# Performance work log

Measured on AMD Instinct MI355X. Metric: run time of the kernel, lower is better.

Reference implementation:

```python
import jax, jax.numpy as jnp
import numpy as np

B, S, D, E, H, K = 4, 2048, 1024, 8, 1024, 2


def setup_inputs() -> dict:
    key = jax.random.key(0)
    k0, k1, k2, k3 = jax.random.split(key, 4)
    x = jax.random.normal(k0, (B, S, D), dtype=jnp.float32)
    router_w = jax.random.normal(k1, (E, D), dtype=jnp.float32) * 0.02
    w1 = jax.random.normal(k2, (D, E * H), dtype=jnp.float32) * 0.02
    w2 = jax.random.normal(k3, (E * H, D), dtype=jnp.float32) * 0.02
    expert_bias = jnp.zeros((E,), dtype=jnp.float32)
    return {"x": x, "router_w": router_w, "w1": w1, "w2": w2, "expert_bias": expert_bias}


def reference(x, router_w, w1, w2, expert_bias):
    b, s, d = x.shape
    e = router_w.shape[0]
    x_flat = x.reshape(-1, d)                      # [T, D]
    T = x_flat.shape[0]

    # Router: sigmoid scores, bias-balanced top-k selection
    router_logits = x_flat @ router_w.T            # [T, E]
    router_probs = jax.nn.sigmoid(router_logits.astype(jnp.float32))
    selection_scores = router_probs + expert_bias[None, :]
    _, selected = jax.lax.top_k(selection_scores, K)          # [T, K] indices
    top_k_w = jnp.take_along_axis(router_probs, selected, axis=-1)
    top_k_w = top_k_w / (top_k_w.sum(-1, keepdims=True) + 1e-20)
    top_k_w = top_k_w.astype(x.dtype)

    # Combine weights as a sparse [T, E] matrix (equivalent to the
    # padded_gather / grouped-GEMM / padded_scatter pipeline since
    # unselected experts get weight 0).
    combine = jnp.zeros((T, e), dtype=x.dtype).at[
        jnp.arange(T)[:, None], selected].add(top_k_w)

    # Expert MLP: relu(x @ w1)^2 @ w2, experts are contiguous column blocks
    h = jnp.square(jax.nn.relu(x_flat @ w1))       # [T, E*H]
    h = h.reshape(T, e, H) * combine[:, :, None]   # weighted per-expert hidden
    y = jnp.einsum('teh,ehd->td', h, w2.reshape(e, H, d))
    output = y.reshape(b, s, d)

    # Aux losses
    router_z_loss = jnp.mean(jnp.square(jax.nn.logsumexp(router_logits, axis=-1)))
    sel_flat = selected.reshape(-1)
    tokens_per_expert = jnp.zeros((e,), jnp.float32).at[sel_flat].add(1.0)
    f_i = (tokens_per_expert / tokens_per_expert.sum()).astype(x.dtype)

    # bias-balancing branch: per-sequence load balance loss
    sel_seq = selected.reshape(b, s * K)
    f_seq = jnp.zeros((b, e), jnp.float32).at[
        jnp.arange(b)[:, None], sel_seq].add(1.0) / (s * K)
    p_seq = router_probs.reshape(b, s, e).mean(axis=1)
    load_balance_loss = e * (f_seq * p_seq).sum(-1).mean()

    # uniform expert widths -> normalized widths are all 1
    widths_norm = jnp.ones((e,), jnp.float32)
    compute_loss = (router_probs @ widths_norm).mean()

    return output, router_z_loss, load_balance_loss, compute_loss, f_i
```

## Files before the change

### kernel.cpp

```cpp
#include <hip/hip_runtime.h>

typedef unsigned short u16;
typedef unsigned int u32;
typedef __bf16 bf16x8 __attribute__((ext_vector_type(8)));
typedef float f32x4 __attribute__((ext_vector_type(4)));

#define NTOK   8192
#define DDIM   1024
#define NEXP   8
#define HDIM   1024
#define PAIRS  16384

__device__ __forceinline__ u16 f2bf(float f) {
  union { float f; u32 u; } v; v.f = f;
  u32 r = v.u + 0x7FFFu + ((v.u >> 16) & 1u);
  return (u16)(r >> 16);
}

__device__ __forceinline__ f32x4 mfma16(bf16x8 a, bf16x8 b, f32x4 c) {
  return __builtin_amdgcn_mfma_f32_16x16x32_bf16(a, b, c, 0, 0, 0);
}

__device__ __forceinline__ void gload16(const void* g, void* l) {
  __builtin_amdgcn_global_load_lds(
      (__attribute__((address_space(1))) void*)g,
      (__attribute__((address_space(3))) void*)l, 16, 0, 0);
}

__global__ __launch_bounds__(256) void transpose_cast(const float* __restrict__ in,
                                                      u16* __restrict__ out,
                                                      int R, int C,
                                                      long in_zs, long out_zs) {
  __shared__ float tile[32][33];
  long ib = (long)blockIdx.z * in_zs;
  long ob = (long)blockIdx.z * out_zs;
  int r0 = blockIdx.y * 32, c0 = blockIdx.x * 32;
  int tx = threadIdx.x & 31, ty = threadIdx.x >> 5;
  #pragma unroll
  for (int rr = 0; rr < 32; rr += 8)
    tile[ty + rr][tx] = in[ib + (long)(r0 + ty + rr) * C + c0 + tx];
  __syncthreads();
  #pragma unroll
  for (int rr = 0; rr < 32; rr += 8)
    out[ob + (long)(c0 + ty + rr) * R + r0 + tx] = f2bf(tile[tx][ty + rr]);
}

__global__ __launch_bounds__(256) void router_kernel(
    const float* __restrict__ x, const float* __restrict__ rw,
    const float* __restrict__ ebias, u16* __restrict__ xb,
    int2* __restrict__ sel, float2* __restrict__ selw,
    float* __restrict__ probs_t, float* __restrict__ lse2_buf,
    u32* __restrict__ cnt, u32* __restrict__ cnt_be) {
  __shared__ float rw_lds[8 * 1028];
  __shared__ double lg[16][8][2];
  __shared__ u32 cl[8];
  int tid = threadIdx.x;
  int tl = tid >> 4, e = (tid >> 1) & 7, s = tid & 1;
  int t = blockIdx.x * 16 + tl;

  for (int i = tid; i < 8192; i += 256)
    rw_lds[(i >> 10) * 1028 + (i & 1023)] = rw[i];
  if (tid < 8) cl[tid] = 0;
  __syncthreads();

  const float* xr = x + (long)t * DDIM;
  const float* wr = rw_lds + e * 1028;
  u16* xbr = xb + (long)t * DDIM;
  double a0 = 0.0, a1 = 0.0;
  int dbase = s * 512;
  for (int d0 = dbase; d0 < dbase + 512; d0 += 16) {
    float4 x0 = *(const float4*)(xr + d0);
    float4 w0 = *(const float4*)(wr + d0);
    float4 x1 = *(const float4*)(xr + d0 + 4);
    float4 w1v = *(const float4*)(wr + d0 + 4);
    float4 x2 = *(const float4*)(xr + d0 + 8);
    float4 w2v = *(const float4*)(wr + d0 + 8);
    float4 x3 = *(const float4*)(xr + d0 + 12);
    float4 w3 = *(const float4*)(wr + d0 + 12);
    a0 += (double)x0.x * w0.x + (double)x0.y * w0.y + (double)x0.z * w0.z + (double)x0.w * w0.w;
    a1 += (double)x1.x * w1v.x + (double)x1.y * w1v.y + (double)x1.z * w1v.z + (double)x1.w * w1v.w;
    a0 += (double)x2.x * w2v.x + (double)x2.y * w2v.y + (double)x2.z * w2v.z + (double)x2.w * w2v.w;
    a1 += (double)x3.x * w3.x + (double)x3.y * w3.y + (double)x3.z * w3.z + (double)x3.w * w3.w;
    if (e == 0) {
      *(ushort4*)(xbr + d0)     = make_ushort4(f2bf(x0.x), f2bf(x0.y), f2bf(x0.z), f2bf(x0.w));
      *(ushort4*)(xbr + d0 + 4) = make_ushort4(f2bf(x1.x), f2bf(x1.y), f2bf(x1.z), f2bf(x1.w));
      *(ushort4*)(xbr + d0 + 8) = make_ushort4(f2bf(x2.x), f2bf(x2.y), f2bf(x2.z), f2bf(x2.w));
      *(ushort4*)(xbr + d0 +12) = make_ushort4(f2bf(x3.x), f2bf(x3.y), f2bf(x3.z), f2bf(x3.w));
    }
  }
  lg[tl][e][s] = a0 + a1;
  __syncthreads();

  if (tid < 16) {
    int t2 = blockIdx.x * 16 + tid;
    double logit[8]; float p[8]; float score[8];
    for (int ee = 0; ee < 8; ee++) {
      logit[ee] = lg[tid][ee][0] + lg[tid][ee][1];
      p[ee] = (float)(1.0 / (1.0 + exp(-logit[ee])));
      score[ee] = p[ee] + ebias[ee];
      probs_t[ee * NTOK + t2] = p[ee];
    }
    int i0 = 0;
    for (int ee = 1; ee < 8; ee++) if (score[ee] > score[i0]) i0 = ee;
    int i1 = (i0 == 0) ? 1 : 0;
    for (int ee = 0; ee < 8; ee++) if (ee != i0 && score[ee] > score[i1]) i1 = ee;
    float w0 = p[i0], w1 = p[i1];
    float ssum = w0 + w1 + 1e-20f;
    sel[t2] = make_int2(i0, i1);
    selw[t2] = make_float2(w0 / ssum, w1 / ssum);
    double m = logit[0];
    for (int ee = 1; ee < 8; ee++) m = fmax(m, logit[ee]);
    double se = 0.0;
    for (int ee = 0; ee < 8; ee++) se += exp(logit[ee] - m);
    double ls = m + log(se);
    lse2_buf[t2] = (float)(ls * ls);
    atomicAdd(&cl[i0], 1u); atomicAdd(&cl[i1], 1u);
  }
  __syncthreads();
  if (tid < 8) {
    int b = (blockIdx.x * 16) >> 11;
    atomicAdd(&cnt[tid], cl[tid]);
    atomicAdd(&cnt_be[b * 8 + tid], cl[tid]);
  }
}

__global__ void offsets_kernel(const u32* __restrict__ cnt, u32* __restrict__ offs,
                               u32* __restrict__ cursor) {
  if (threadIdx.x == 0 && blockIdx.x == 0) {
    u32 a = 0;
    for (int e = 0; e < 8; e++) { offs[e] = a; cursor[e] = a; a += cnt[e]; }
  }
}

__global__ __launch_bounds__(256) void build_lists(
    const int2* __restrict__ sel, const float2* __restrict__ selw,
    u32* __restrict__ cursor, int* __restrict__ tok_list, float* __restrict__ wt_list,
    int* __restrict__ inv) {
  int t = blockIdx.x * 256 + threadIdx.x;
  int2 s = sel[t]; float2 w = selw[t];
  u32 p0 = atomicAdd(&cursor[s.x], 1u);
  tok_list[p0] = t; wt_list[p0] = w.x; inv[2 * t] = (int)p0;
  u32 p1 = atomicAdd(&cursor[s.y], 1u);
  tok_list[p1] = t; wt_list[p1] = w.y; inv[2 * t + 1] = (int)p1;
}

template <bool SECOND>
__global__ __launch_bounds__(256) void moe_gemm(
    const u16* __restrict__ A, const u16* __restrict__ Bt,
    u16* __restrict__ out16,
    const int* __restrict__ tok_list, const float* __restrict__ wt_list,
    const u32* __restrict__ cnt, const u32* __restrict__ offs) {
  int tn = blockIdx.x & 7;
  int tm = blockIdx.x >> 3;
  int e = 0, acct = 0;
  while (e < 8) {
    int nt = (int)((cnt[e] + 127u) >> 7);
    if (tm < acct + nt) break;
    acct += nt; e++;
  }
  if (e == 8) return;
  int m0 = (tm - acct) * 128;
  int off = (int)offs[e];
  int ce  = (int)cnt[e];

  __shared__ uint4 As[1024];
  __shared__ uint4 Bs[1024];

  int tid = threadIdx.x;
  int l = tid & 63, w = tid >> 6;

  const u16* agp[4]; const u16* bgp[4];
  #pragma unroll
  for (int j = 0; j < 4; j++) {
    int p = w * 256 + j * 64 + l;
    int row = p >> 3, c = p & 7;
    long arow;
    if (SECOND) {
      arow = (long)(off + m0 + row);
    } else {
      int rr = m0 + row; if (rr > ce - 1) rr = ce - 1;
      arow = (long)tok_list[off + rr];
    }
    agp[j] = A + arow * 1024 + c * 8;
    bgp[j] = Bt + (long)e * 1048576 + (long)(tn * 128 + row) * 1024 + c * 8;
  }

  f32x4 acc[4][4];
  #pragma unroll
  for (int i = 0; i < 4; i++)
    #pragma unroll
    for (int j = 0; j < 4; j++) acc[i][j] = (f32x4){0.f, 0.f, 0.f, 0.f};

  int mr = l & 15, q = l >> 4;
  int wm = (w >> 1) * 64, wn = (w & 1) * 64;

  for (int k0 = 0; k0 < 1024; k0 += 64) {
    #pragma unroll
    for (int j = 0; j < 4; j++) {
      gload16(agp[j], &As[w * 256 + j * 64]);
      gload16(bgp[j], &Bs[w * 256 + j * 64]);
      agp[j] += 64; bgp[j] += 64;
    }
    __syncthreads();
    #pragma unroll
    for (int kk = 0; kk < 2; kk++) {
      int cg = kk * 4 + q;
      bf16x8 af[4], bfr[4];
      #pragma unroll
      for (int i = 0; i < 4; i++) {
        af[i]  = __builtin_bit_cast(bf16x8, As[(wm + i * 16 + mr) * 8 + cg]);
        bfr[i] = __builtin_bit_cast(bf16x8, Bs[(wn + i * 16 + mr) * 8 + cg]);
      }
      #pragma unroll
      for (int i = 0; i < 4; i++)
        #pragma unroll
        for (int j = 0; j < 4; j++)
          acc[i][j] = mfma16(af[i], bfr[j], acc[i][j]);
    }
    __syncthreads();
  }

  #pragma unroll
  for (int i = 0; i < 4; i++) {
    #pragma unroll
    for (int r = 0; r < 4; r++) {
      int rr = wm + i * 16 + q * 4 + r;
      if (m0 + rr >= ce) continue;
      int slot = off + m0 + rr;
      float wgt = SECOND ? wt_list[slot] : 0.f;
      #pragma unroll
      for (int j = 0; j < 4; j++) {
        int cc = tn * 128 + wn + j * 16 + mr;
        float v = acc[i][j][r];
        if (!SECOND) {
          v = fmaxf(v, 0.f); v = v * v;
          out16[(long)slot * 1024 + cc] = f2bf(v);
        } else {
          out16[(long)slot * 1024 + cc] = f2bf(v * wgt);
        }
      }
    }
  }
}

__global__ __launch_bounds__(128) void combine_kernel(
    const u16* __restrict__ y, const int* __restrict__ inv,
    float* __restrict__ out) {
  int t = blockIdx.x, tid = threadIdx.x;
  int s0 = inv[2 * t], s1 = inv[2 * t + 1];
  uint4 a = *(const uint4*)(y + (long)s0 * 1024 + tid * 8);
  uint4 b = *(const uint4*)(y + (long)s1 * 1024 + tid * 8);
  float o[8];
  const u32* au = (const u32*)&a;
  const u32* bu = (const u32*)&b;
  #pragma unroll
  for (int i = 0; i < 4; i++) {
    union { u32 u; float f; } lo1, hi1, lo2, hi2;
    lo1.u = au[i] << 16;  hi1.u = au[i] & 0xFFFF0000u;
    lo2.u = bu[i] << 16;  hi2.u = bu[i] & 0xFFFF0000u;
    o[2 * i]     = lo1.f + lo2.f;
    o[2 * i + 1] = hi1.f + hi2.f;
  }
  float* op = out + (long)t * 1024 + tid * 8;
  *(float4*)op       = make_float4(o[0], o[1], o[2], o[3]);
  *(float4*)(op + 4) = make_float4(o[4], o[5], o[6], o[7]);
}

__global__ __launch_bounds__(256) void reduce_pe(
    const float* __restrict__ probs_t, const float* __restrict__ lse2,
    float* __restrict__ pe_sum, float* __restrict__ z_part) {
  __shared__ float sd[256];
  int tid = threadIdx.x, blk = blockIdx.x;
  float s = 0.f;
  if (blk < 32) {
    int b = blk >> 3, e = blk & 7;
    const float* p = probs_t + e * NTOK + b * 2048;
    for (int i = tid; i < 2048; i += 256) s += p[i];
  } else {
    const float* p = lse2 + (blk - 32) * 1024;
    for (int i = tid; i < 1024; i += 256) s += p[i];
  }
  sd[tid] = s; __syncthreads();
  for (int st = 128; st > 0; st >>= 1) {
    if (tid < st) sd[tid] += sd[tid + st];
    __syncthreads();
  }
  if (tid == 0) {
    if (blk < 32) pe_sum[blk] = sd[0];
    else z_part[blk - 32] = sd[0];
  }
}

__global__ void finalize_kernel(
    const float* __restrict__ pe_sum, const float* __restrict__ z_part,
    const u32* __restrict__ cnt, const u32* __restrict__ cnt_be,
    float* __restrict__ out_tail) {
  if (threadIdx.x == 0 && blockIdx.x == 0) {
    float z = 0.f;
    for (int i = 0; i < 8; i++) z += z_part[i];
    z /= (float)NTOK;
    float lb = 0.f, clv = 0.f;
    for (int p = 0; p < 32; p++) {
      float psum = pe_sum[p];
      clv += psum;
      float f = (float)cnt_be[p] / 4096.0f;
      lb += f * (psum / 2048.0f);
    }
    lb = 8.0f * lb / 4.0f;
    clv = clv / (float)NTOK;
    out_tail[0] = z;
    out_tail[1] = lb;
    out_tail[2] = clv;
    for (int e2 = 0; e2 < 8; e2++) out_tail[3 + e2] = (float)cnt[e2] / 16384.0f;
  }
}

extern "C" void kernel_launch(void* const* d_in, const int* in_sizes, int n_in,
                              void* d_out, int out_size, void* d_ws, size_t ws_size,
                              hipStream_t stream) {
  const float* x     = (const float*)d_in[0];
  const float* rw    = (const float*)d_in[1];
  const float* w1    = (const float*)d_in[2];
  const float* w2    = (const float*)d_in[3];
  const float* ebias = (const float*)d_in[4];
  float* out = (float*)d_out;

  char* ws = (char*)d_ws;
  u16*    xb        = (u16*)(ws + 0);
  u16*    w1t       = (u16*)(ws + 16777216);
  u16*    y         = (u16*)(ws + 0);
  u16*    w2t       = (u16*)(ws + 33554432);
  u16*    h         = (u16*)(ws + 50331648);
  int*    tok_list  = (int*)(ws + 84148224);
  float*  wt_list   = (float*)(ws + 84213760);
  int2*   sel       = (int2*)(ws + 84279296);
  float2* selw      = (float2*)(ws + 84344832);
  float*  probs_t   = (float*)(ws + 84410368);
  float*  lse2_buf  = (float*)(ws + 84672512);
  int*    inv       = (int*)(ws + 84705280);
  u32*    cnt       = (u32*)(ws + 84770816);
  u32*    cursor    = cnt + 8;
  u32*    cnt_be    = cnt + 16;
  u32*    offs      = cnt + 48;
  float*  pe_sum    = (float*)(cnt + 56);
  float*  z_part    = (float*)(cnt + 88);

  hipMemsetAsync(cnt, 0, 512, stream);

  transpose_cast<<<dim3(256, 32, 1), 256, 0, stream>>>(w1, w1t, 1024, 8192, 0, 0);
  transpose_cast<<<dim3(32, 32, 8), 256, 0, stream>>>(w2, w2t, 1024, 1024, 1048576L, 1048576L);
  router_kernel<<<512, 256, 0, stream>>>(x, rw, ebias, xb, sel, selw, probs_t, lse2_buf, cnt, cnt_be);
  offsets_kernel<<<1, 64, 0, stream>>>(cnt, offs, cursor);
  build_lists<<<32, 256, 0, stream>>>(sel, selw, cursor, tok_list, wt_list, inv);
  moe_gemm<false><<<136 * 8, 256, 0, stream>>>(xb, w1t, h, tok_list, wt_list, cnt, offs);
  moe_gemm<true><<<136 * 8, 256, 0, stream>>>(h, w2t, y, tok_list, wt_list, cnt, offs);
  combine_kernel<<<8192, 128, 0, stream>>>(y, inv, out);
  reduce_pe<<<40, 256, 0, stream>>>(probs_t, lse2_buf, pe_sum, z_part);
  finalize_kernel<<<1, 64, 0, stream>>>(pe_sum, z_part, cnt, cnt_be, out + 8388608);
}
```

Before: 420.7 us.

## Double-buffer MoE GEMM, stage epilogue stores, fuse router reductions and transposes

The MoE GEMM now double-buffers its A/B tiles in LDS so the next K-slice loads while the current one computes. It also stages the output tile through LDS so global writes are coalesced 16-byte stores, and sets launch bounds to two blocks per CU. The router is reorganised to one 32-lane group per token and reduces the per-expert probability sums and z-loss in-kernel with atomics, which removes the probs/lse buffers and the reduce_pe kernel. The two weight-transpose launches are merged into one. The changes add LDS pressure and float atomics whose summation order is nondeterministic.

```diff
diff --git a/kernel.cpp b/kernel.cpp
--- a/kernel.cpp
+++ b/kernel.cpp
@@ -27,101 +27,100 @@
       (__attribute__((address_space(3))) void*)l, 16, 0, 0);
 }
 
-__global__ __launch_bounds__(256) void transpose_cast(const float* __restrict__ in,
-                                                      u16* __restrict__ out,
-                                                      int R, int C,
-                                                      long in_zs, long out_zs) {
+__global__ __launch_bounds__(256) void transpose_all(
+    const float* __restrict__ w1, const float* __restrict__ w2,
+    u16* __restrict__ w1t, u16* __restrict__ w2t) {
   __shared__ float tile[32][33];
-  long ib = (long)blockIdx.z * in_zs;
-  long ob = (long)blockIdx.z * out_zs;
+  int z = blockIdx.z;
+  const float* ib; long rs; u16* ob;
+  if (z < 8) { ib = w1 + z * 1024; rs = 8192; ob = w1t + (long)z * 1048576; }
+  else       { ib = w2 + (long)(z - 8) * 1048576; rs = 1024; ob = w2t + (long)(z - 8) * 1048576; }
   int r0 = blockIdx.y * 32, c0 = blockIdx.x * 32;
   int tx = threadIdx.x & 31, ty = threadIdx.x >> 5;
   #pragma unroll
   for (int rr = 0; rr < 32; rr += 8)
-    tile[ty + rr][tx] = in[ib + (long)(r0 + ty + rr) * C + c0 + tx];
+    tile[ty + rr][tx] = ib[(long)(r0 + ty + rr) * rs + c0 + tx];
   __syncthreads();
   #pragma unroll
   for (int rr = 0; rr < 32; rr += 8)
-    out[ob + (long)(c0 + ty + rr) * R + r0 + tx] = f2bf(tile[tx][ty + rr]);
+    ob[(long)(c0 + ty + rr) * 1024 + r0 + tx] = f2bf(tile[tx][ty + rr]);
 }
 
 __global__ __launch_bounds__(256) void router_kernel(
     const float* __restrict__ x, const float* __restrict__ rw,
     const float* __restrict__ ebias, u16* __restrict__ xb,
     int2* __restrict__ sel, float2* __restrict__ selw,
-    float* __restrict__ probs_t, float* __restrict__ lse2_buf,
-    u32* __restrict__ cnt, u32* __restrict__ cnt_be) {
+    u32* __restrict__ cnt, u32* __restrict__ cnt_be,
+    float* __restrict__ pe_sum, float* __restrict__ z_sum) {
   __shared__ float rw_lds[8 * 1028];
-  __shared__ double lg[16][8][2];
+  __shared__ float pe_loc[8];
+  __shared__ float z_loc;
   __shared__ u32 cl[8];
   int tid = threadIdx.x;
-  int tl = tid >> 4, e = (tid >> 1) & 7, s = tid & 1;
-  int t = blockIdx.x * 16 + tl;
-
   for (int i = tid; i < 8192; i += 256)
     rw_lds[(i >> 10) * 1028 + (i & 1023)] = rw[i];
-  if (tid < 8) cl[tid] = 0;
+  if (tid < 8) { pe_loc[tid] = 0.f; cl[tid] = 0u; }
+  if (tid == 8) z_loc = 0.f;
   __syncthreads();
 
+  int ht = tid >> 5;
+  int hl = tid & 31;
+  int t = blockIdx.x * 8 + ht;
   const float* xr = x + (long)t * DDIM;
-  const float* wr = rw_lds + e * 1028;
   u16* xbr = xb + (long)t * DDIM;
-  double a0 = 0.0, a1 = 0.0;
-  int dbase = s * 512;
-  for (int d0 = dbase; d0 < dbase + 512; d0 += 16) {
-    float4 x0 = *(const float4*)(xr + d0);
-    float4 w0 = *(const float4*)(wr + d0);
-    float4 x1 = *(const float4*)(xr + d0 + 4);
-    float4 w1v = *(const float4*)(wr + d0 + 4);
-    float4 x2 = *(const float4*)(xr + d0 + 8);
-    float4 w2v = *(const float4*)(wr + d0 + 8);
-    float4 x3 = *(const float4*)(xr + d0 + 12);
-    float4 w3 = *(const float4*)(wr + d0 + 12);
-    a0 += (double)x0.x * w0.x + (double)x0.y * w0.y + (double)x0.z * w0.z + (double)x0.w * w0.w;
-    a1 += (double)x1.x * w1v.x + (double)x1.y * w1v.y + (double)x1.z * w1v.z + (double)x1.w * w1v.w;
-    a0 += (double)x2.x * w2v.x + (double)x2.y * w2v.y + (double)x2.z * w2v.z + (double)x2.w * w2v.w;
-    a1 += (double)x3.x * w3.x + (double)x3.y * w3.y + (double)x3.z * w3.z + (double)x3.w * w3.w;
-    if (e == 0) {
-      *(ushort4*)(xbr + d0)     = make_ushort4(f2bf(x0.x), f2bf(x0.y), f2bf(x0.z), f2bf(x0.w));
-      *(ushort4*)(xbr + d0 + 4) = make_ushort4(f2bf(x1.x), f2bf(x1.y), f2bf(x1.z), f2bf(x1.w));
-      *(ushort4*)(xbr + d0 + 8) = make_ushort4(f2bf(x2.x), f2bf(x2.y), f2bf(x2.z), f2bf(x2.w));
-      *(ushort4*)(xbr + d0 +12) = make_ushort4(f2bf(x3.x), f2bf(x3.y), f2bf(x3.z), f2bf(x3.w));
-    }
-  }
-  lg[tl][e][s] = a0 + a1;
-  __syncthreads();
-
-  if (tid < 16) {
-    int t2 = blockIdx.x * 16 + tid;
-    double logit[8]; float p[8]; float score[8];
-    for (int ee = 0; ee < 8; ee++) {
-      logit[ee] = lg[tid][ee][0] + lg[tid][ee][1];
-      p[ee] = (float)(1.0 / (1.0 + exp(-logit[ee])));
-      score[ee] = p[ee] + ebias[ee];
-      probs_t[ee * NTOK + t2] = p[ee];
+  double acc[8];
+  #pragma unroll
+  for (int e = 0; e < 8; e++) acc[e] = 0.0;
+  #pragma unroll
+  for (int p = 0; p < 8; p++) {
+    int d = p * 128 + hl * 4;
+    float4 xv = *(const float4*)(xr + d);
+    *(ushort4*)(xbr + d) = make_ushort4(f2bf(xv.x), f2bf(xv.y), f2bf(xv.z), f2bf(xv.w));
+    #pragma unroll
+    for (int e = 0; e < 8; e++) {
+      float4 wv = *(const float4*)(rw_lds + e * 1028 + d);
+      acc[e] += (double)xv.x * (double)wv.x + (double)xv.y * (double)wv.y
+              + (double)xv.z * (double)wv.z + (double)xv.w * (double)wv.w;
+    }
+  }
+  #pragma unroll
+  for (int e = 0; e < 8; e++) {
+    #pragma unroll
+    for (int off = 16; off > 0; off >>= 1)
+      acc[e] += __shfl_down(acc[e], off, 32);
+  }
+  if (hl == 0) {
+    double logit[8]; float p8[8], score[8];
+    for (int e = 0; e < 8; e++) {
+      logit[e] = acc[e];
+      p8[e] = (float)(1.0 / (1.0 + exp(-logit[e])));
+      score[e] = p8[e] + ebias[e];
     }
     int i0 = 0;
-    for (int ee = 1; ee < 8; ee++) if (score[ee] > score[i0]) i0 = ee;
+    for (int e = 1; e < 8; e++) if (score[e] > score[i0]) i0 = e;
     int i1 = (i0 == 0) ? 1 : 0;
-    for (int ee = 0; ee < 8; ee++) if (ee != i0 && score[ee] > score[i1]) i1 = ee;
-    float w0 = p[i0], w1 = p[i1];
-    float ssum = w0 + w1 + 1e-20f;
-    sel[t2] = make_int2(i0, i1);
-    selw[t2] = make_float2(w0 / ssum, w1 / ssum);
+    for (int e = 0; e < 8; e++) if (e != i0 && score[e] > score[i1]) i1 = e;
+    float w0 = p8[i0], w1v = p8[i1];
+    float ssum = w0 + w1v + 1e-20f;
+    sel[t] = make_int2(i0, i1);
+    selw[t] = make_float2(w0 / ssum, w1v / ssum);
     double m = logit[0];
-    for (int ee = 1; ee < 8; ee++) m = fmax(m, logit[ee]);
+    for (int e = 1; e < 8; e++) m = fmax(m, logit[e]);
     double se = 0.0;
-    for (int ee = 0; ee < 8; ee++) se += exp(logit[ee] - m);
+    for (int e = 0; e < 8; e++) se += exp(logit[e] - m);
     double ls = m + log(se);
-    lse2_buf[t2] = (float)(ls * ls);
+    atomicAdd(&z_loc, (float)(ls * ls));
+    for (int e = 0; e < 8; e++) atomicAdd(&pe_loc[e], p8[e]);
     atomicAdd(&cl[i0], 1u); atomicAdd(&cl[i1], 1u);
   }
   __syncthreads();
   if (tid < 8) {
-    int b = (blockIdx.x * 16) >> 11;
+    int b = (int)((blockIdx.x * 8) >> 11);
     atomicAdd(&cnt[tid], cl[tid]);
     atomicAdd(&cnt_be[b * 8 + tid], cl[tid]);
-  }
+    atomicAdd(&pe_sum[b * 8 + tid], pe_loc[tid]);
+  }
+  if (tid == 8) atomicAdd(z_sum, z_loc);
 }
 
 __global__ void offsets_kernel(const u32* __restrict__ cnt, u32* __restrict__ offs,
@@ -145,7 +144,7 @@
 }
 
 template <bool SECOND>
-__global__ __launch_bounds__(256) void moe_gemm(
+__global__ __launch_bounds__(256, 2) void moe_gemm(
     const u16* __restrict__ A, const u16* __restrict__ Bt,
     u16* __restrict__ out16,
     const int* __restrict__ tok_list, const float* __restrict__ wt_list,
@@ -163,8 +162,7 @@
   int off = (int)offs[e];
   int ce  = (int)cnt[e];
 
-  __shared__ uint4 As[1024];
-  __shared__ uint4 Bs[1024];
+  __shared__ uint4 smem[4096];
 
   int tid = threadIdx.x;
   int l = tid & 63, w = tid >> 6;
@@ -185,6 +183,14 @@
     bgp[j] = Bt + (long)e * 1048576 + (long)(tn * 128 + row) * 1024 + c * 8;
   }
 
+  #pragma unroll
+  for (int j = 0; j < 4; j++) {
+    gload16(agp[j], &smem[w * 256 + j * 64]);
+    gload16(bgp[j], &smem[2048 + w * 256 + j * 64]);
+    agp[j] += 64; bgp[j] += 64;
+  }
+  __syncthreads();
+
   f32x4 acc[4][4];
   #pragma unroll
   for (int i = 0; i < 4; i++)
@@ -194,22 +200,26 @@
   int mr = l & 15, q = l >> 4;
   int wm = (w >> 1) * 64, wn = (w & 1) * 64;
 
-  for (int k0 = 0; k0 < 1024; k0 += 64) {
-    #pragma unroll
-    for (int j = 0; j < 4; j++) {
-      gload16(agp[j], &As[w * 256 + j * 64]);
-      gload16(bgp[j], &Bs[w * 256 + j * 64]);
-      agp[j] += 64; bgp[j] += 64;
-    }
-    __syncthreads();
+  for (int k = 0; k < 16; k++) {
+    int cur = k & 1, nxt = cur ^ 1;
+    if (k < 15) {
+      #pragma unroll
+      for (int j = 0; j < 4; j++) {
+        gload16(agp[j], &smem[nxt * 1024 + w * 256 + j * 64]);
+        gload16(bgp[j], &smem[2048 + nxt * 1024 + w * 256 + j * 64]);
+        agp[j] += 64; bgp[j] += 64;
+      }
+    }
+    const uint4* Ab = smem + cur * 1024;
+    const uint4* Bb = smem + 2048 + cur * 1024;
     #pragma unroll
     for (int kk = 0; kk < 2; kk++) {
       int cg = kk * 4 + q;
       bf16x8 af[4], bfr[4];
       #pragma unroll
       for (int i = 0; i < 4; i++) {
-        af[i]  = __builtin_bit_cast(bf16x8, As[(wm + i * 16 + mr) * 8 + cg]);
-        bfr[i] = __builtin_bit_cast(bf16x8, Bs[(wn + i * 16 + mr) * 8 + cg]);
+        af[i]  = __builtin_bit_cast(bf16x8, Ab[(wm + i * 16 + mr) * 8 + cg]);
+        bfr[i] = __builtin_bit_cast(bf16x8, Bb[(wn + i * 16 + mr) * 8 + cg]);
       }
       #pragma unroll
       for (int i = 0; i < 4; i++)
@@ -220,26 +230,35 @@
     __syncthreads();
   }
 
+  u16* ost = (u16*)smem + w * 4608;
   #pragma unroll
   for (int i = 0; i < 4; i++) {
     #pragma unroll
     for (int r = 0; r < 4; r++) {
-      int rr = wm + i * 16 + q * 4 + r;
-      if (m0 + rr >= ce) continue;
-      int slot = off + m0 + rr;
-      float wgt = SECOND ? wt_list[slot] : 0.f;
+      int rl = i * 16 + q * 4 + r;
+      float wgt = 1.f;
+      if (SECOND) {
+        int gr = m0 + wm + rl;
+        int slot = (gr < ce) ? (off + gr) : 0;
+        wgt = wt_list[slot];
+      }
       #pragma unroll
       for (int j = 0; j < 4; j++) {
-        int cc = tn * 128 + wn + j * 16 + mr;
         float v = acc[i][j][r];
-        if (!SECOND) {
-          v = fmaxf(v, 0.f); v = v * v;
-          out16[(long)slot * 1024 + cc] = f2bf(v);
-        } else {
-          out16[(long)slot * 1024 + cc] = f2bf(v * wgt);
-        }
+        if (!SECOND) { v = fmaxf(v, 0.f); v = v * v; }
+        else v *= wgt;
+        ost[rl * 72 + j * 16 + mr] = f2bf(v);
       }
     }
+  }
+  #pragma unroll
+  for (int pr = 0; pr < 8; pr++) {
+    int rl = pr * 8 + (l >> 3);
+    int c8 = l & 7;
+    uint4 v = *(const uint4*)(ost + rl * 72 + c8 * 8);
+    int gr = m0 + wm + rl;
+    if (gr < ce)
+      *(uint4*)(out16 + (long)(off + gr) * 1024 + tn * 128 + wn + c8 * 8) = v;
   }
 }
 
@@ -266,39 +285,12 @@
   *(float4*)(op + 4) = make_float4(o[4], o[5], o[6], o[7]);
 }
 
-__global__ __launch_bounds__(256) void reduce_pe(
-    const float* __restrict__ probs_t, const float* __restrict__ lse2,
-    float* __restrict__ pe_sum, float* __restrict__ z_part) {
-  __shared__ float sd[256];
-  int tid = threadIdx.x, blk = blockIdx.x;
-  float s = 0.f;
-  if (blk < 32) {
-    int b = blk >> 3, e = blk & 7;
-    const float* p = probs_t + e * NTOK + b * 2048;
-    for (int i = tid; i < 2048; i += 256) s += p[i];
-  } else {
-    const float* p = lse2 + (blk - 32) * 1024;
-    for (int i = tid; i < 1024; i += 256) s += p[i];
-  }
-  sd[tid] = s; __syncthreads();
-  for (int st = 128; st > 0; st >>= 1) {
-    if (tid < st) sd[tid] += sd[tid + st];
-    __syncthreads();
-  }
-  if (tid == 0) {
-    if (blk < 32) pe_sum[blk] = sd[0];
-    else z_part[blk - 32] = sd[0];
-  }
-}
-
 __global__ void finalize_kernel(
-    const float* __restrict__ pe_sum, const float* __restrict__ z_part,
+    const float* __restrict__ pe_sum, const float* __restrict__ z_sum,
     const u32* __restrict__ cnt, const u32* __restrict__ cnt_be,
     float* __restrict__ out_tail) {
   if (threadIdx.x == 0 && blockIdx.x == 0) {
-    float z = 0.f;
-    for (int i = 0; i < 8; i++) z += z_part[i];
-    z /= (float)NTOK;
+    float z = z_sum[0] / (float)NTOK;
     float lb = 0.f, clv = 0.f;
     for (int p = 0; p < 32; p++) {
       float psum = pe_sum[p];
@@ -335,26 +327,22 @@
   float*  wt_list   = (float*)(ws + 84213760);
   int2*   sel       = (int2*)(ws + 84279296);
   float2* selw      = (float2*)(ws + 84344832);
-  float*  probs_t   = (float*)(ws + 84410368);
-  float*  lse2_buf  = (float*)(ws + 84672512);
   int*    inv       = (int*)(ws + 84705280);
   u32*    cnt       = (u32*)(ws + 84770816);
   u32*    cursor    = cnt + 8;
   u32*    cnt_be    = cnt + 16;
   u32*    offs      = cnt + 48;
   float*  pe_sum    = (float*)(cnt + 56);
-  float*  z_part    = (float*)(cnt + 88);
+  float*  z_sum     = (float*)(cnt + 88);
 
   hipMemsetAsync(cnt, 0, 512, stream);
 
-  transpose_cast<<<dim3(256, 32, 1), 256, 0, stream>>>(w1, w1t, 1024, 8192, 0, 0);
-  transpose_cast<<<dim3(32, 32, 8), 256, 0, stream>>>(w2, w2t, 1024, 1024, 1048576L, 1048576L);
-  router_kernel<<<512, 256, 0, stream>>>(x, rw, ebias, xb, sel, selw, probs_t, lse2_buf, cnt, cnt_be);
+  transpose_all<<<dim3(32, 32, 16), 256, 0, stream>>>(w1, w2, w1t, w2t);
+  router_kernel<<<1024, 256, 0, stream>>>(x, rw, ebias, xb, sel, selw, cnt, cnt_be, pe_sum, z_sum);
   offsets_kernel<<<1, 64, 0, stream>>>(cnt, offs, cursor);
   build_lists<<<32, 256, 0, stream>>>(sel, selw, cursor, tok_list, wt_list, inv);
   moe_gemm<false><<<136 * 8, 256, 0, stream>>>(xb, w1t, h, tok_list, wt_list, cnt, offs);
   moe_gemm<true><<<136 * 8, 256, 0, stream>>>(h, w2t, y, tok_list, wt_list, cnt, offs);
   combine_kernel<<<8192, 128, 0, stream>>>(y, inv, out);
-  reduce_pe<<<40, 256, 0, stream>>>(probs_t, lse2_buf, pe_sum, z_part);
-  finalize_kernel<<<1, 64, 0, stream>>>(pe_sum, z_part, cnt, cnt_be, out + 8388608);
-}
+  finalize_kernel<<<1, 64, 0, stream>>>(pe_sum, z_sum, cnt, cnt_be, out + 8388608);
+}
```

New measurement: 376.6 us. -10.5%, faster.
